# Optimization experiments

Measured on AMD Instinct MI355X. Metric: run time of the kernel, lower is better.

## Reference

```python
import jax, jax.numpy as jnp
import numpy as np

N, E, F_IN, H, H2, G, C = 30000, 480000, 1280, 512, 256, 64, 10


def _linear_init(key, fan_in, fan_out):
    k1, k2 = jax.random.split(key)
    s = 1.0 / np.sqrt(fan_in)
    W = jax.random.uniform(k1, (fan_in, fan_out), jnp.float32, -s, s)
    b = jax.random.uniform(k2, (fan_out,), jnp.float32, -s, s)
    return W, b


def setup_inputs() -> dict:
    key = jax.random.key(0)
    ks = jax.random.split(key, 6)
    x = jax.random.normal(ks[0], (N, F_IN), jnp.float32)
    edge_index = jax.random.randint(ks[1], (2, E), 0, N, dtype=jnp.int32).astype(jnp.int64)
    batch = jnp.sort(jax.random.randint(ks[2], (N,), 0, G, dtype=jnp.int32)).astype(jnp.int64)
    W1, b1 = _linear_init(ks[3], F_IN, H)
    beta2 = jnp.ones((), jnp.float32)  # AGNNConv beta init = 1.0 (trainable in prop2)
    W2, b2 = _linear_init(ks[4], H, H2)
    W3, b3 = _linear_init(ks[5], 2 * H2, C)
    return {"x": x, "edge_index": edge_index, "batch": batch,
            "W1": W1, "b1": b1, "beta2": beta2,
            "W2": W2, "b2": b2, "W3": W3, "b3": b3}


def _agnn(x, src, dst, beta, n):
    # L2 normalize (PyG F.normalize: clamp norm at 1e-12)
    norm = jnp.maximum(jnp.linalg.norm(x, axis=-1, keepdims=True), 1e-12)
    xn = x / norm
    # per-edge cosine similarity attention logits
    alpha = beta * jnp.sum(xn[src] * xn[dst], axis=-1)  # [E']
    # softmax over incoming edges of each destination node
    amax = jax.ops.segment_max(alpha, dst, num_segments=n)
    ex = jnp.exp(alpha - amax[dst])
    denom = jax.ops.segment_sum(ex, dst, num_segments=n)
    w = ex / denom[dst]
    # weighted scatter-add of raw source features
    return jax.ops.segment_sum(w[:, None] * x[src], dst, num_segments=n)


def reference(x, edge_index, batch, W1, b1, beta2, W2, b2, W3, b3):
    n = x.shape[0]
    h = jax.nn.relu(x @ W1 + b1)  # [N, 512]
    # AGNNConv adds self-loops by default
    loops = jnp.arange(n, dtype=edge_index.dtype)
    src = jnp.concatenate([edge_index[0], loops])
    dst = jnp.concatenate([edge_index[1], loops])
    h = _agnn(h, src, dst, jnp.float32(1.0), n)  # prop1: fixed beta=1
    h = _agnn(h, src, dst, beta2, n)             # prop2: learned beta
    h = jax.nn.relu(h @ W2 + b2)  # [N, 256]
    # global max / mean pool per graph
    gmx = jax.ops.segment_max(h, batch, num_segments=G)
    cnt = jnp.maximum(jax.ops.segment_sum(jnp.ones((n,), h.dtype), batch, num_segments=G), 1.0)
    gav = jax.ops.segment_sum(h, batch, num_segments=G) / cnt[:, None]
    return jnp.concatenate([gmx, gav], axis=1) @ W3 + b3  # [G, C]
```

## Files before the change

kernel.cpp:

```cpp
#include <hip/hip_runtime.h>
#include <hip/hip_bf16.h>
#include <cstdint>


typedef __attribute__((ext_vector_type(8))) short bf16x8;
typedef __attribute__((ext_vector_type(4))) float f32x4;
typedef __attribute__((ext_vector_type(8))) unsigned short ushort8;
typedef __attribute__((ext_vector_type(4))) unsigned short ushort4v;
typedef __attribute__((ext_vector_type(4))) unsigned int uint4v;

__device__ inline unsigned short f2bf(float f) {
    unsigned int u = __float_as_uint(f);
    u += 0x7FFFu + ((u >> 16) & 1u);
    return (unsigned short)(u >> 16);
}

__device__ __forceinline__ float bf2f(unsigned short u) {
    return __uint_as_float(((unsigned int)u) << 16);
}

__device__ __forceinline__ unsigned int cvtpk(float lo, float hi) {
    unsigned int r;
    asm("v_cvt_pk_bf16_f32 %0, %1, %2" : "=v"(r) : "v"(lo), "v"(hi));
    return r;
}

__device__ __forceinline__ void gload_lds16(const void* g, void* l) {
    __builtin_amdgcn_global_load_lds(
        (const __attribute__((address_space(1))) void*)g,
        (__attribute__((address_space(3))) void*)l, 16, 0, 0);
}

__device__ __forceinline__ float wave_sum_dpp(float p) {
    int t;
    t = __builtin_amdgcn_update_dpp(0, __float_as_int(p), 0xB1, 0xf, 0xf, true);
    p += __int_as_float(t);
    t = __builtin_amdgcn_update_dpp(0, __float_as_int(p), 0x4E, 0xf, 0xf, true);
    p += __int_as_float(t);
    t = __builtin_amdgcn_update_dpp(0, __float_as_int(p), 0x141, 0xf, 0xf, true);
    p += __int_as_float(t);
    t = __builtin_amdgcn_update_dpp(0, __float_as_int(p), 0x140, 0xf, 0xf, true);
    p += __int_as_float(t);
    t = __builtin_amdgcn_update_dpp(0, __float_as_int(p), 0x142, 0xf, 0xf, true);
    p += __int_as_float(t);
    t = __builtin_amdgcn_update_dpp(0, __float_as_int(p), 0x143, 0xf, 0xf, true);
    p += __int_as_float(t);
    return __int_as_float(__builtin_amdgcn_readlane(__float_as_int(p), 63));
}

__global__ __launch_bounds__(256) void k_transpose_bf16(
    const float* __restrict__ W, unsigned short* __restrict__ Wt, int K, int N) {
    __shared__ unsigned short t[32][33];
    int k0 = blockIdx.x * 32, n0 = blockIdx.y * 32;
    int tr = threadIdx.x >> 3;
    int tc = (threadIdx.x & 7) * 4;
    float4 v = *(const float4*)(W + (long)(k0 + tr) * N + n0 + tc);
    t[tr][tc + 0] = f2bf(v.x); t[tr][tc + 1] = f2bf(v.y);
    t[tr][tc + 2] = f2bf(v.z); t[tr][tc + 3] = f2bf(v.w);
    __syncthreads();
    ushort4v o = { t[tc + 0][tr], t[tc + 1][tr], t[tc + 2][tr], t[tc + 3][tr] };
    *(ushort4v*)(Wt + (long)(n0 + tr) * K + k0 + tc) = o;
}

template <int K, int BN, int NOUT, bool AF32, bool OUTBF16>
__global__ __launch_bounds__(512, 4) void k_gemm_bias_relu(
    const void* __restrict__ Av, const unsigned short* __restrict__ Bt,
    const float* __restrict__ bias, void* __restrict__ Cv, int M) {
    __shared__ unsigned short As[2][128 * 32];
    __shared__ unsigned short Bs[2][BN * 32];
    int tid = threadIdx.x;
    int w = tid >> 6, l = tid & 63;
    int wm = w >> 2, wn = w & 3;
    int mBase = blockIdx.x * 128;
    int nBase = blockIdx.y * BN;

    const float* Af = (const float*)Av;
    const unsigned short* Ab = (const unsigned short*)Av;

    int arow = tid >> 2;
    int aslot = (tid & 3) ^ ((arow >> 1) & 3);
    long aRowG = mBase + arow; if (aRowG >= M) aRowG = M - 1;
    const float* aptr = AF32 ? (Af + aRowG * K + (tid & 3) * 8) : nullptr;

    auto stageB = [&](int b, int k0) {
#pragma unroll
        for (int o = 0; o < BN / 128; ++o) {
            int rbase = (w * (BN / 128) + o) * 16;
            int row = rbase + (l >> 2);
            int gsrc = (l & 3) ^ ((row >> 1) & 3);
            gload_lds16(Bt + (long)(nBase + row) * K + k0 + gsrc * 8,
                        &Bs[b][rbase * 32]);
        }
    };
    auto stageAbf = [&](int b, int k0) {
        int rbase = w * 16;
        int row = rbase + (l >> 2);
        int gsrc = (l & 3) ^ ((row >> 1) & 3);
        long gr = mBase + row; if (gr >= M) gr = M - 1;
        gload_lds16(Ab + gr * K + k0 + gsrc * 8, &As[b][rbase * 32]);
    };

    f32x4 acc[4][4] = {};
    constexpr int NSTEP = K / 32;

    stageB(0, 0);
    if constexpr (AF32) {
        float4 f0 = *(const float4*)(aptr);
        float4 f1 = *(const float4*)(aptr + 4);
        uint4v p = { cvtpk(f0.x, f0.y), cvtpk(f0.z, f0.w),
                     cvtpk(f1.x, f1.y), cvtpk(f1.z, f1.w) };
        *(uint4v*)(&As[0][arow * 32 + aslot * 8]) = p;
    } else {
        stageAbf(0, 0);
    }
    __syncthreads();

    int s = 0;
    for (int step = 0; step < NSTEP; ++step, s ^= 1) {
        int nk = (step + 1) * 32;
        float4 f0, f1;
        if (nk < K) {
            stageB(s ^ 1, nk);
            if constexpr (AF32) {
                f0 = *(const float4*)(aptr + nk);
                f1 = *(const float4*)(aptr + nk + 4);
            } else {
                stageAbf(s ^ 1, nk);
            }
        }
        bf16x8 af[4];
#pragma unroll
        for (int m = 0; m < 4; ++m) {
            int ra = wm * 64 + m * 16 + (l & 15);
            int g = (l >> 4) ^ ((ra >> 1) & 3);
            af[m] = *(const bf16x8*)(&As[s][ra * 32 + g * 8]);
        }
#pragma unroll
        for (int n = 0; n < 4; ++n) {
            int rb = wn * 64 + n * 16 + (l & 15);
            int g = (l >> 4) ^ ((rb >> 1) & 3);
            bf16x8 bfr = *(const bf16x8*)(&Bs[s][rb * 32 + g * 8]);
#pragma unroll
            for (int m = 0; m < 4; ++m)
                acc[m][n] = __builtin_amdgcn_mfma_f32_16x16x32_bf16(
                    af[m], bfr, acc[m][n], 0, 0, 0);
        }
        if constexpr (AF32) {
            if (nk < K) {
                uint4v p = { cvtpk(f0.x, f0.y), cvtpk(f0.z, f0.w),
                             cvtpk(f1.x, f1.y), cvtpk(f1.z, f1.w) };
                *(uint4v*)(&As[s ^ 1][arow * 32 + aslot * 8]) = p;
            }
        }
        __syncthreads();
    }

#pragma unroll
    for (int m = 0; m < 4; ++m) {
        int row = mBase + wm * 64 + m * 16 + (l >> 4) * 4;
#pragma unroll
        for (int n = 0; n < 4; ++n) {
            int colg = nBase + wn * 64 + n * 16 + (l & 15);
            float bv = bias[colg];
#pragma unroll
            for (int r = 0; r < 4; ++r) {
                if (row + r < M) {
                    float v = fmaxf(acc[m][n][r] + bv, 0.f);
                    if constexpr (OUTBF16)
                        ((unsigned short*)Cv)[(long)(row + r) * NOUT + colg] = f2bf(v);
                    else
                        ((float*)Cv)[(long)(row + r) * NOUT + colg] = v;
                }
            }
        }
    }
}

__global__ void k_csr_init(int* __restrict__ cnt, int* __restrict__ fill, int n) {
    int i = blockIdx.x * blockDim.x + threadIdx.x;
    if (i < n) { cnt[i] = 1; fill[i] = 0; }
}

__global__ void k_csr_count(const int* __restrict__ ei, int* __restrict__ cnt, int E) {
    int e = blockIdx.x * blockDim.x + threadIdx.x;
    if (e < E) atomicAdd(&cnt[ei[E + e]], 1);
}

__global__ __launch_bounds__(1024) void k_scan1(const int* __restrict__ cnt,
                                                int* __restrict__ rowp,
                                                int* __restrict__ bsum, int n) {
    __shared__ int wsum[16];
    int b = blockIdx.x, t = threadIdx.x, lane = t & 63, w = t >> 6;
    int i = b * 1024 + t;
    int v = (i < n) ? cnt[i] : 0;
    int x = v;
#pragma unroll
    for (int off = 1; off < 64; off <<= 1) {
        int y = __shfl_up(x, off, 64);
        if (lane >= off) x += y;
    }
    if (lane == 63) wsum[w] = x;
    __syncthreads();
    if (t < 16) {
        int s = wsum[t];
#pragma unroll
        for (int off = 1; off < 16; off <<= 1) {
            int y = __shfl_up(s, off, 64);
            if (t >= off) s += y;
        }
        wsum[t] = s;
    }
    __syncthreads();
    int wo = w ? wsum[w - 1] : 0;
    if (i < n) rowp[i] = wo + x - v;
    if (t == 0) bsum[b] = wsum[15];
}

__global__ __launch_bounds__(64) void k_scan2(int* __restrict__ bsum, int nb) {
    int lane = threadIdx.x;
    int v = (lane < nb) ? bsum[lane] : 0;
    int x = v;
#pragma unroll
    for (int off = 1; off < 64; off <<= 1) {
        int y = __shfl_up(x, off, 64);
        if (lane >= off) x += y;
    }
    int total = __shfl(x, nb - 1, 64);
    if (lane < nb) bsum[lane] = x - v;
    if (lane == 0) bsum[nb] = total;
}

__global__ __launch_bounds__(1024) void k_scan3(const int* __restrict__ bsum,
                                                int* __restrict__ rowp, int n, int nb) {
    int i = blockIdx.x * 1024 + threadIdx.x;
    if (i < n) rowp[i] += bsum[i >> 10];
    else if (i == n) rowp[n] = bsum[nb];
}

__global__ void k_csr_fill(const int* __restrict__ ei, const int* __restrict__ rowp,
                           int* __restrict__ fill, int* __restrict__ col, int E, int n) {
    int idx = blockIdx.x * blockDim.x + threadIdx.x;
    if (idx < E) {
        int d = ei[E + idx];
        int s = ei[idx];
        int pos = atomicAdd(&fill[d], 1);
        col[rowp[d] + pos] = s;
    } else if (idx < E + n) {
        int nd = idx - E;
        int pos = atomicAdd(&fill[nd], 1);
        col[rowp[nd] + pos] = nd;
    }
}

__global__ __launch_bounds__(256) void k_norm_bf16(const unsigned short* __restrict__ h,
                                                   float* __restrict__ invn, int n) {
    int row = blockIdx.x * 4 + (threadIdx.x >> 6);
    int lane = threadIdx.x & 63;
    if (row >= n) return;
    ushort8 v = *(const ushort8*)(h + (long)row * 512 + lane * 8);
    float s = 0.f;
#pragma unroll
    for (int e = 0; e < 8; ++e) { float f = bf2f(v[e]); s += f * f; }
    s = wave_sum_dpp(s);
    if (lane == 0) invn[row] = 1.f / fmaxf(sqrtf(s), 1e-12f);
}

__global__ __launch_bounds__(256) void k_agnn(
    const unsigned short* __restrict__ h, const float* __restrict__ invn,
    const int* __restrict__ rowp, const int* __restrict__ col,
    const float* __restrict__ beta_ptr, unsigned short* __restrict__ out,
    float* __restrict__ invn_out, int nNodes) {
    int dst = blockIdx.x * 4 + (threadIdx.x >> 6);
    int lane = threadIdx.x & 63;
    if (dst >= nNodes) return;
    float beta = beta_ptr ? beta_ptr[0] : 1.0f;
    ushort8 hdv = *(const ushort8*)(h + (long)dst * 512 + lane * 8);
    float hd[8];
#pragma unroll
    for (int e = 0; e < 8; ++e) hd[e] = bf2f(hdv[e]);
    float coef = beta * invn[dst];
    int s0 = rowp[dst], s1 = rowp[dst + 1];

    float m = -1e30f, ssum = 0.f;
    float acc[8] = {0.f, 0.f, 0.f, 0.f, 0.f, 0.f, 0.f, 0.f};

    for (int base = s0; base < s1; base += 64) {
        int cnt = min(s1 - base, 64);
        int gi = base + lane; if (gi >= s1) gi = s1 - 1;
        int idxl = col[gi];
        float vinl = invn[idxl];
        int src0 = __builtin_amdgcn_readlane(idxl, 0);
        ushort8 nxt = *(const ushort8*)(h + (long)src0 * 512 + lane * 8);
        for (int j = 0; j < cnt; ++j) {
            ushort8 cur = nxt;
            if (j + 1 < cnt) {
                int sn = __builtin_amdgcn_readlane(idxl, j + 1);
                nxt = *(const ushort8*)(h + (long)sn * 512 + lane * 8);
            }
            float a[8];
#pragma unroll
            for (int e = 0; e < 8; ++e) a[e] = bf2f(cur[e]);
            float p = a[0] * hd[0] + a[1] * hd[1] + a[2] * hd[2] + a[3] * hd[3] +
                      a[4] * hd[4] + a[5] * hd[5] + a[6] * hd[6] + a[7] * hd[7];
            p = wave_sum_dpp(p);
            float vin_j = __int_as_float(
                __builtin_amdgcn_readlane(__float_as_int(vinl), j));
            float alpha = coef * vin_j * p;
            if (alpha > m) {
                float sc = __expf(m - alpha);
                ssum *= sc;
#pragma unroll
                for (int e = 0; e < 8; ++e) acc[e] *= sc;
                m = alpha;
            }
            float wgt = __expf(alpha - m);
            ssum += wgt;
#pragma unroll
            for (int e = 0; e < 8; ++e) acc[e] += wgt * a[e];
        }
    }
    float inv_s = 1.f / ssum;
#pragma unroll
    for (int e = 0; e < 8; ++e) acc[e] *= inv_s;

    uint4v o = { cvtpk(acc[0], acc[1]), cvtpk(acc[2], acc[3]),
                 cvtpk(acc[4], acc[5]), cvtpk(acc[6], acc[7]) };
    *(uint4v*)(out + (long)dst * 512 + lane * 8) = o;

    if (invn_out) {
        float s = 0.f;
#pragma unroll
        for (int e = 0; e < 8; ++e) s += acc[e] * acc[e];
        s = wave_sum_dpp(s);
        if (lane == 0) invn_out[dst] = 1.f / fmaxf(sqrtf(s), 1e-12f);
    }
}

__global__ void k_bounds(const int* __restrict__ batch, int* __restrict__ starts,
                         int n, int G) {
    int g = blockIdx.x * blockDim.x + threadIdx.x;
    if (g > G) return;
    int lo = 0, hi = n;
    while (lo < hi) {
        int mid = (lo + hi) >> 1;
        if (batch[mid] < g) lo = mid + 1; else hi = mid;
    }
    starts[g] = lo;
}

__global__ __launch_bounds__(256) void k_pool(const float* __restrict__ h3,
                                              const int* __restrict__ starts,
                                              float* __restrict__ pooled) {
    int g = blockIdx.x;
    int t = threadIdx.x;
    int s = starts[g], e = starts[g + 1];
    float mx = -3.402823466e38f, sm = 0.f;
    int r = s;
    for (; r + 4 <= e; r += 4) {
        float v0 = h3[(long)(r + 0) * 256 + t];
        float v1 = h3[(long)(r + 1) * 256 + t];
        float v2 = h3[(long)(r + 2) * 256 + t];
        float v3 = h3[(long)(r + 3) * 256 + t];
        mx = fmaxf(mx, fmaxf(fmaxf(v0, v1), fmaxf(v2, v3)));
        sm += (v0 + v1) + (v2 + v3);
    }
    for (; r < e; ++r) {
        float v = h3[(long)r * 256 + t];
        mx = fmaxf(mx, v); sm += v;
    }
    float cnt = fmaxf((float)(e - s), 1.f);
    pooled[g * 512 + t] = mx;
    pooled[g * 512 + 256 + t] = sm / cnt;
}

__global__ __launch_bounds__(64) void k_final(const float* __restrict__ pooled,
                                              const float* __restrict__ W3,
                                              const float* __restrict__ b3,
                                              float* __restrict__ out, int C) {
    int g = blockIdx.x;
    int lane = threadIdx.x;
    for (int c = 0; c < C; c++) {
        float p = 0.f;
        for (int k = lane; k < 512; k += 64) p += pooled[g * 512 + k] * W3[k * C + c];
#pragma unroll
        for (int off = 32; off; off >>= 1) p += __shfl_xor(p, off, 64);
        if (lane == 0) out[g * C + c] = p + b3[c];
    }
}

extern "C" void kernel_launch(void* const* d_in, const int* in_sizes, int n_in,
                              void* d_out, int out_size, void* d_ws, size_t ws_size,
                              hipStream_t stream) {
    const float* x     = (const float*)d_in[0];
    const int*   ei    = (const int*)d_in[1];
    const int*   batch = (const int*)d_in[2];
    const float* W1    = (const float*)d_in[3];
    const float* b1    = (const float*)d_in[4];
    const float* beta2 = (const float*)d_in[5];
    const float* W2    = (const float*)d_in[6];
    const float* b2    = (const float*)d_in[7];
    const float* W3    = (const float*)d_in[8];
    const float* b3    = (const float*)d_in[9];
    float* out = (float*)d_out;

    const int N = in_sizes[2];
    const int E = in_sizes[1] / 2;
    const int F_IN = in_sizes[0] / N;
    const int H = in_sizes[4];
    const int H2 = in_sizes[7];
    const int C = in_sizes[9];
    const int G = out_size / C;

    char* ws = (char*)d_ws;
    unsigned short* H1B = (unsigned short*)(ws + 0);
    unsigned short* HPB = (unsigned short*)(ws + 31000000L);
    unsigned short* H2B = (unsigned short*)(ws + 62000000L);
    float*          H3  = (float*)(ws + 0);
    unsigned short* W1T = (unsigned short*)(ws + 93000000L);
    unsigned short* W2T = (unsigned short*)(ws + 94500000L);
    float* INVN_A = (float*)(ws + 95000000L);
    float* INVN_B = (float*)(ws + 95200000L);
    int*   CNT    = (int*)(ws + 95400000L);
    int*   FILL   = (int*)(ws + 95600000L);
    int*   ROWP   = (int*)(ws + 95800000L);
    int*   COL    = (int*)(ws + 96000000L);
    int*   BSUM   = (int*)(ws + 98100000L);
    int*   START  = (int*)(ws + 98110000L);
    float* POOLED = (float*)(ws + 98120000L);

    { dim3 g1(F_IN / 32, H / 32); k_transpose_bf16<<<g1, 256, 0, stream>>>(W1, W1T, F_IN, H); }
    { dim3 g2(H / 32, H2 / 32);   k_transpose_bf16<<<g2, 256, 0, stream>>>(W2, W2T, H, H2); }

    int nb = (N + 1023) / 1024;
    k_csr_init<<<(N + 255) / 256, 256, 0, stream>>>(CNT, FILL, N);
    k_csr_count<<<(E + 255) / 256, 256, 0, stream>>>(ei, CNT, E);
    k_scan1<<<nb, 1024, 0, stream>>>(CNT, ROWP, BSUM, N);
    k_scan2<<<1, 64, 0, stream>>>(BSUM, nb);
    k_scan3<<<(N + 1 + 1023) / 1024, 1024, 0, stream>>>(BSUM, ROWP, N, nb);
    k_csr_fill<<<(E + N + 255) / 256, 256, 0, stream>>>(ei, ROWP, FILL, COL, E, N);

    {
        dim3 grid((N + 127) / 128, H / 256);
        k_gemm_bias_relu<1280, 256, 512, true, true>
            <<<grid, 512, 0, stream>>>(x, W1T, b1, H1B, N);
    }

    k_norm_bf16<<<(N + 3) / 4, 256, 0, stream>>>(H1B, INVN_A, N);
    k_agnn<<<(N + 3) / 4, 256, 0, stream>>>(H1B, INVN_A, ROWP, COL, nullptr, HPB, INVN_B, N);

    k_agnn<<<(N + 3) / 4, 256, 0, stream>>>(HPB, INVN_B, ROWP, COL, beta2, H2B, nullptr, N);

    {
        dim3 grid((N + 127) / 128, 1);
        k_gemm_bias_relu<512, 256, 256, false, false>
            <<<grid, 512, 0, stream>>>(H2B, W2T, b2, H3, N);
    }

    k_bounds<<<1, 128, 0, stream>>>(batch, START, N, G);
    k_pool<<<G, 256, 0, stream>>>(H3, START, POOLED);
    k_final<<<G, 64, 0, stream>>>(POOLED, W3, b3, out, C);
}
```

Baseline: 376.2 us.

## Triple-buffer GEMM LDS staging with manual vmcnt waits and prefetch depth two

Changes the bias+ReLU GEMM from double to triple buffering in LDS. Global loads are issued two K-steps ahead, and the A data is held in registers across one extra step. Explicit s_waitcnt vmcnt counts and raw s_barrier replace __syncthreads so that memory latency can overlap the MFMA work. The cost is 50% more LDS, which may lower occupancy under launch_bounds(512,4). The hand-counted vmcnt values also risk race bugs if they do not match the real number of loads in flight.

```diff
diff --git a/kernel.cpp b/kernel.cpp
--- a/kernel.cpp
+++ b/kernel.cpp
@@ -8,6 +8,9 @@
 typedef __attribute__((ext_vector_type(8))) unsigned short ushort8;
 typedef __attribute__((ext_vector_type(4))) unsigned short ushort4v;
 typedef __attribute__((ext_vector_type(4))) unsigned int uint4v;
+
+#define WAITV(n) asm volatile("s_waitcnt vmcnt(" #n ")" ::: "memory")
+#define WAITLGKM asm volatile("s_waitcnt lgkmcnt(0)" ::: "memory")
 
 __device__ inline unsigned short f2bf(float f) {
     unsigned int u = __float_as_uint(f);
@@ -66,8 +69,9 @@
 __global__ __launch_bounds__(512, 4) void k_gemm_bias_relu(
     const void* __restrict__ Av, const unsigned short* __restrict__ Bt,
     const float* __restrict__ bias, void* __restrict__ Cv, int M) {
-    __shared__ unsigned short As[2][128 * 32];
-    __shared__ unsigned short Bs[2][BN * 32];
+    constexpr int NS = K / 32;
+    __shared__ unsigned short As[3][128 * 32];
+    __shared__ unsigned short Bs[3][BN * 32];
     int tid = threadIdx.x;
     int w = tid >> 6, l = tid & 63;
     int wm = w >> 2, wn = w & 3;
@@ -99,60 +103,76 @@
         long gr = mBase + row; if (gr >= M) gr = M - 1;
         gload_lds16(Ab + gr * K + k0 + gsrc * 8, &As[b][rbase * 32]);
     };
+    auto loadA = [&](int k0, float4& u0, float4& u1) {
+        u0 = *(const float4*)(aptr + k0);
+        u1 = *(const float4*)(aptr + k0 + 4);
+    };
+    auto writeA = [&](int b, float4 u0, float4 u1) {
+        uint4v p = { cvtpk(u0.x, u0.y), cvtpk(u0.z, u0.w),
+                     cvtpk(u1.x, u1.y), cvtpk(u1.z, u1.w) };
+        *(uint4v*)(&As[b][arow * 32 + aslot * 8]) = p;
+    };
 
     f32x4 acc[4][4] = {};
-    constexpr int NSTEP = K / 32;
-
-    stageB(0, 0);
+    float4 curA0 = {}, curA1 = {}, nxtA0 = {}, nxtA1 = {};
+
     if constexpr (AF32) {
-        float4 f0 = *(const float4*)(aptr);
-        float4 f1 = *(const float4*)(aptr + 4);
-        uint4v p = { cvtpk(f0.x, f0.y), cvtpk(f0.z, f0.w),
-                     cvtpk(f1.x, f1.y), cvtpk(f1.z, f1.w) };
-        *(uint4v*)(&As[0][arow * 32 + aslot * 8]) = p;
+        float4 z0, z1;
+        loadA(0, z0, z1);
+        stageB(0, 0);
+        loadA(32, curA0, curA1);
+        stageB(1, 32);
+        writeA(0, z0, z1);
     } else {
-        stageAbf(0, 0);
-    }
-    __syncthreads();
-
-    int s = 0;
-    for (int step = 0; step < NSTEP; ++step, s ^= 1) {
-        int nk = (step + 1) * 32;
-        float4 f0, f1;
-        if (nk < K) {
-            stageB(s ^ 1, nk);
-            if constexpr (AF32) {
-                f0 = *(const float4*)(aptr + nk);
-                f1 = *(const float4*)(aptr + nk + 4);
-            } else {
-                stageAbf(s ^ 1, nk);
-            }
-        }
+        stageAbf(0, 0); stageB(0, 0);
+        stageAbf(1, 32); stageB(1, 32);
+    }
+    WAITLGKM;
+
+#pragma unroll
+    for (int t = 0; t < NS; ++t) {
+        const int cb = t % 3, nb = (t + 1) % 3, fb = (t + 2) % 3;
+        __builtin_amdgcn_s_barrier();
+        __builtin_amdgcn_sched_barrier(0);
+        if constexpr (AF32) {
+            if (t + 2 < NS) {
+                loadA((t + 2) * 32, nxtA0, nxtA1);
+                stageB(fb, (t + 2) * 32);
+            }
+            if (t + 1 < NS) {
+                writeA(nb, curA0, curA1);
+                curA0 = nxtA0; curA1 = nxtA1;
+            }
+            if (t < NS - 2) { WAITV(6); }
+            else if (t == NS - 2) { WAITV(2); }
+            else { WAITV(0); }
+        } else {
+            if (t + 2 < NS) {
+                stageAbf(fb, (t + 2) * 32);
+                stageB(fb, (t + 2) * 32);
+            }
+            if (t < NS - 2) { WAITV(6); }
+            else if (t == NS - 2) { WAITV(3); }
+            else { WAITV(0); }
+        }
+        __builtin_amdgcn_sched_barrier(0);
         bf16x8 af[4];
 #pragma unroll
         for (int m = 0; m < 4; ++m) {
             int ra = wm * 64 + m * 16 + (l & 15);
             int g = (l >> 4) ^ ((ra >> 1) & 3);
-            af[m] = *(const bf16x8*)(&As[s][ra * 32 + g * 8]);
+            af[m] = *(const bf16x8*)(&As[cb][ra * 32 + g * 8]);
         }
 #pragma unroll
         for (int n = 0; n < 4; ++n) {
             int rb = wn * 64 + n * 16 + (l & 15);
             int g = (l >> 4) ^ ((rb >> 1) & 3);
-            bf16x8 bfr = *(const bf16x8*)(&Bs[s][rb * 32 + g * 8]);
+            bf16x8 bfr = *(const bf16x8*)(&Bs[cb][rb * 32 + g * 8]);
 #pragma unroll
             for (int m = 0; m < 4; ++m)
                 acc[m][n] = __builtin_amdgcn_mfma_f32_16x16x32_bf16(
                     af[m], bfr, acc[m][n], 0, 0, 0);
         }
-        if constexpr (AF32) {
-            if (nk < K) {
-                uint4v p = { cvtpk(f0.x, f0.y), cvtpk(f0.z, f0.w),
-                             cvtpk(f1.x, f1.y), cvtpk(f1.z, f1.w) };
-                *(uint4v*)(&As[s ^ 1][arow * 32 + aslot * 8]) = p;
-            }
-        }
-        __syncthreads();
     }
 
 #pragma unroll
```

After: 375.3 us. About the same (-0.2%).

## Use fixed softmax shift in AGNN, unroll gathers 2x with deeper prefetch, prefetch GEMM A further

Applied to the files above, without the earlier changes.

The AGNN kernel drops the online-max softmax rescaling and uses a fixed shift of |beta|*1.0625. This relies on cosine-similarity logits being bounded by |beta|. The edge loop is unrolled by two with separate even/odd accumulators and a four-deep gather prefetch, so more memory loads are in flight and the per-edge branch goes away. The fp32-A GEMM path now prefetches A two k-steps ahead in registers to hide global load latency. The fixed shift stays mathematically valid because alpha is bounded by |beta|, but at the cost of a little extra register pressure.

```diff
diff --git a/kernel.cpp b/kernel.cpp
--- a/kernel.cpp
+++ b/kernel.cpp
@@ -66,6 +66,7 @@
 __global__ __launch_bounds__(512, 4) void k_gemm_bias_relu(
     const void* __restrict__ Av, const unsigned short* __restrict__ Bt,
     const float* __restrict__ bias, void* __restrict__ Cv, int M) {
+    constexpr int NSTEP = K / 32;
     __shared__ unsigned short As[2][128 * 32];
     __shared__ unsigned short Bs[2][BN * 32];
     int tid = threadIdx.x;
@@ -101,15 +102,19 @@
     };
 
     f32x4 acc[4][4] = {};
-    constexpr int NSTEP = K / 32;
+    float4 Aw0 = {}, Aw1 = {}, An0 = {}, An1 = {};
 
     stageB(0, 0);
     if constexpr (AF32) {
-        float4 f0 = *(const float4*)(aptr);
-        float4 f1 = *(const float4*)(aptr + 4);
-        uint4v p = { cvtpk(f0.x, f0.y), cvtpk(f0.z, f0.w),
-                     cvtpk(f1.x, f1.y), cvtpk(f1.z, f1.w) };
+        float4 z0 = *(const float4*)(aptr);
+        float4 z1 = *(const float4*)(aptr + 4);
+        uint4v p = { cvtpk(z0.x, z0.y), cvtpk(z0.z, z0.w),
+                     cvtpk(z1.x, z1.y), cvtpk(z1.z, z1.w) };
         *(uint4v*)(&As[0][arow * 32 + aslot * 8]) = p;
+        if (NSTEP > 1) {
+            Aw0 = *(const float4*)(aptr + 32);
+            Aw1 = *(const float4*)(aptr + 36);
+        }
     } else {
         stageAbf(0, 0);
     }
@@ -118,14 +123,15 @@
     int s = 0;
     for (int step = 0; step < NSTEP; ++step, s ^= 1) {
         int nk = (step + 1) * 32;
-        float4 f0, f1;
+        int nk2 = (step + 2) * 32;
         if (nk < K) {
             stageB(s ^ 1, nk);
-            if constexpr (AF32) {
-                f0 = *(const float4*)(aptr + nk);
-                f1 = *(const float4*)(aptr + nk + 4);
-            } else {
-                stageAbf(s ^ 1, nk);
+            if constexpr (!AF32) stageAbf(s ^ 1, nk);
+        }
+        if constexpr (AF32) {
+            if (nk2 < K) {
+                An0 = *(const float4*)(aptr + nk2);
+                An1 = *(const float4*)(aptr + nk2 + 4);
             }
         }
         bf16x8 af[4];
@@ -147,9 +153,10 @@
         }
         if constexpr (AF32) {
             if (nk < K) {
-                uint4v p = { cvtpk(f0.x, f0.y), cvtpk(f0.z, f0.w),
-                             cvtpk(f1.x, f1.y), cvtpk(f1.z, f1.w) };
+                uint4v p = { cvtpk(Aw0.x, Aw0.y), cvtpk(Aw0.z, Aw0.w),
+                             cvtpk(Aw1.x, Aw1.y), cvtpk(Aw1.z, Aw1.w) };
                 *(uint4v*)(&As[s ^ 1][arow * 32 + aslot * 8]) = p;
+                Aw0 = An0; Aw1 = An1;
             }
         }
         __syncthreads();
@@ -279,49 +286,64 @@
 #pragma unroll
     for (int e = 0; e < 8; ++e) hd[e] = bf2f(hdv[e]);
     float coef = beta * invn[dst];
+    float mshift = fabsf(beta) * 1.0625f;
     int s0 = rowp[dst], s1 = rowp[dst + 1];
 
-    float m = -1e30f, ssum = 0.f;
-    float acc[8] = {0.f, 0.f, 0.f, 0.f, 0.f, 0.f, 0.f, 0.f};
+    float ssum = 0.f;
+    float accE[8] = {0.f, 0.f, 0.f, 0.f, 0.f, 0.f, 0.f, 0.f};
+    float accO[8] = {0.f, 0.f, 0.f, 0.f, 0.f, 0.f, 0.f, 0.f};
 
     for (int base = s0; base < s1; base += 64) {
         int cnt = min(s1 - base, 64);
         int gi = base + lane; if (gi >= s1) gi = s1 - 1;
         int idxl = col[gi];
         float vinl = invn[idxl];
-        int src0 = __builtin_amdgcn_readlane(idxl, 0);
-        ushort8 nxt = *(const ushort8*)(h + (long)src0 * 512 + lane * 8);
-        for (int j = 0; j < cnt; ++j) {
-            ushort8 cur = nxt;
-            if (j + 1 < cnt) {
-                int sn = __builtin_amdgcn_readlane(idxl, j + 1);
-                nxt = *(const ushort8*)(h + (long)sn * 512 + lane * 8);
-            }
-            float a[8];
-#pragma unroll
-            for (int e = 0; e < 8; ++e) a[e] = bf2f(cur[e]);
-            float p = a[0] * hd[0] + a[1] * hd[1] + a[2] * hd[2] + a[3] * hd[3] +
-                      a[4] * hd[4] + a[5] * hd[5] + a[6] * hd[6] + a[7] * hd[7];
-            p = wave_sum_dpp(p);
-            float vin_j = __int_as_float(
-                __builtin_amdgcn_readlane(__float_as_int(vinl), j));
-            float alpha = coef * vin_j * p;
-            if (alpha > m) {
-                float sc = __expf(m - alpha);
-                ssum *= sc;
-#pragma unroll
-                for (int e = 0; e < 8; ++e) acc[e] *= sc;
-                m = alpha;
-            }
-            float wgt = __expf(alpha - m);
-            ssum += wgt;
-#pragma unroll
-            for (int e = 0; e < 8; ++e) acc[e] += wgt * a[e];
+        ushort8 r0 = {}, r1 = {}, r2 = {}, r3 = {};
+        r0 = *(const ushort8*)(h + (long)__builtin_amdgcn_readlane(idxl, 0) * 512 + lane * 8);
+        if (cnt > 1) r1 = *(const ushort8*)(h + (long)__builtin_amdgcn_readlane(idxl, 1) * 512 + lane * 8);
+        if (cnt > 2) r2 = *(const ushort8*)(h + (long)__builtin_amdgcn_readlane(idxl, 2) * 512 + lane * 8);
+        if (cnt > 3) r3 = *(const ushort8*)(h + (long)__builtin_amdgcn_readlane(idxl, 3) * 512 + lane * 8);
+        int j = 0;
+        for (; j + 1 < cnt; j += 2) {
+            ushort8 c0 = r0, c1 = r1;
+            r0 = r2; r1 = r3;
+            if (j + 4 < cnt) r2 = *(const ushort8*)(h + (long)__builtin_amdgcn_readlane(idxl, j + 4) * 512 + lane * 8);
+            if (j + 5 < cnt) r3 = *(const ushort8*)(h + (long)__builtin_amdgcn_readlane(idxl, j + 5) * 512 + lane * 8);
+            float a0[8], a1[8];
+#pragma unroll
+            for (int e = 0; e < 8; ++e) { a0[e] = bf2f(c0[e]); a1[e] = bf2f(c1[e]); }
+            float p0 = a0[0] * hd[0] + a0[1] * hd[1] + a0[2] * hd[2] + a0[3] * hd[3] +
+                       a0[4] * hd[4] + a0[5] * hd[5] + a0[6] * hd[6] + a0[7] * hd[7];
+            float p1 = a1[0] * hd[0] + a1[1] * hd[1] + a1[2] * hd[2] + a1[3] * hd[3] +
+                       a1[4] * hd[4] + a1[5] * hd[5] + a1[6] * hd[6] + a1[7] * hd[7];
+            p0 = wave_sum_dpp(p0);
+            p1 = wave_sum_dpp(p1);
+            float al0 = coef * __int_as_float(__builtin_amdgcn_readlane(__float_as_int(vinl), j)) * p0;
+            float al1 = coef * __int_as_float(__builtin_amdgcn_readlane(__float_as_int(vinl), j + 1)) * p1;
+            float w0 = __expf(al0 - mshift);
+            float w1 = __expf(al1 - mshift);
+            ssum += w0 + w1;
+#pragma unroll
+            for (int e = 0; e < 8; ++e) { accE[e] += w0 * a0[e]; accO[e] += w1 * a1[e]; }
+        }
+        if (j < cnt) {
+            float a0[8];
+#pragma unroll
+            for (int e = 0; e < 8; ++e) a0[e] = bf2f(r0[e]);
+            float p0 = a0[0] * hd[0] + a0[1] * hd[1] + a0[2] * hd[2] + a0[3] * hd[3] +
+                       a0[4] * hd[4] + a0[5] * hd[5] + a0[6] * hd[6] + a0[7] * hd[7];
+            p0 = wave_sum_dpp(p0);
+            float al0 = coef * __int_as_float(__builtin_amdgcn_readlane(__float_as_int(vinl), j)) * p0;
+            float w0 = __expf(al0 - mshift);
+            ssum += w0;
+#pragma unroll
+            for (int e = 0; e < 8; ++e) accE[e] += w0 * a0[e];
         }
     }
     float inv_s = 1.f / ssum;
-#pragma unroll
-    for (int e = 0; e < 8; ++e) acc[e] *= inv_s;
+    float acc[8];
+#pragma unroll
+    for (int e = 0; e < 8; ++e) acc[e] = (accE[e] + accO[e]) * inv_s;
 
     uint4v o = { cvtpk(acc[0], acc[1]), cvtpk(acc[2], acc[3]),
                  cvtpk(acc[4], acc[5]), cvtpk(acc[6], acc[7]) };
```

Measured after the change: 379.3 us. About the same (+0.8%).
